# Performance work log

Hardware: AMD Instinct MI355X
Metric: run time of the kernel (lower is better)

## Reference

```python
import jax, jax.numpy as jnp
import numpy as np

N = 50000      # nodes
E = 800000     # edges (before self-loops)
D = 128        # input_dim
H = 128        # hidden_dim
G = 256        # graphs in batch


def setup_inputs() -> dict:
    key = jax.random.key(0)
    ks = jax.random.split(key, 6)
    x = jax.random.normal(ks[0], (N, D), dtype=jnp.float32)
    edge_index = jax.random.randint(ks[1], (2, E), 0, N, dtype=jnp.int32)
    batch = jnp.sort(jax.random.randint(ks[2], (N,), 0, G, dtype=jnp.int32))
    W1 = jax.random.normal(ks[3], (D, H), dtype=jnp.float32) / np.sqrt(D).astype(np.float32)
    b1 = jnp.zeros((H,), jnp.float32)
    W2 = jax.random.normal(ks[4], (H, H), dtype=jnp.float32) / np.sqrt(H).astype(np.float32)
    b2 = jnp.zeros((H,), jnp.float32)
    alpha = jnp.full((H,), 0.25, jnp.float32)  # PReLU(hidden_dim) init
    return dict(x=x, edge_index=edge_index, batch=batch,
                W1=W1, b1=b1, W2=W2, b2=b2, alpha=alpha)


def _gcn_layer(z, W, b, src, dst, norm):
    # GCNConv: z' = D^{-1/2}(A+I)D^{-1/2} (z W) + b
    zw = z @ W                                            # [N,H] dense GEMM
    agg = jnp.zeros_like(zw).at[dst].add(norm[:, None] * zw[src])  # scatter-add over edges
    return agg + b


def reference(x, edge_index, batch, W1, b1, W2, b2, alpha):
    loop = jnp.arange(N, dtype=edge_index.dtype)
    src = jnp.concatenate([edge_index[0], loop])          # add self-loops
    dst = jnp.concatenate([edge_index[1], loop])
    deg = jnp.zeros((N,), x.dtype).at[dst].add(jnp.float32(1.0))
    dinv = jnp.where(deg > 0, jax.lax.rsqrt(deg), 0.0)
    norm = dinv[src] * dinv[dst]                          # [E+N] edge weights

    zs = []
    z = x
    for (W, b) in ((W1, b1), (W2, b2)):
        z = _gcn_layer(z, W, b, src, dst, norm)
        z = jnp.where(z > 0, z, alpha * z)                # channel-wise PReLU (shared)
        zs.append(z)

    gs = [jax.ops.segment_sum(zi, batch, num_segments=G) for zi in zs]  # global_add_pool
    g = jnp.concatenate(gs, axis=1)                       # [G, num_layers*H]
    return z, g
```

## Files before the change

### kernel.cpp

```cpp
#include <hip/hip_runtime.h>
#include <stdint.h>


#define CAP 96

typedef __attribute__((ext_vector_type(8))) short short8;
typedef __attribute__((ext_vector_type(4))) float f32x4;

__device__ __forceinline__ uint16_t bf16rne(float f) {
    uint32_t u = __float_as_uint(f);
    uint32_t r = (u + 0x7fffu + ((u >> 16) & 1u)) >> 16;
    return (uint16_t)r;
}
__device__ __forceinline__ float bf_lo(uint32_t v) { return __uint_as_float(v << 16); }
__device__ __forceinline__ float bf_hi(uint32_t v) { return __uint_as_float(v & 0xffff0000u); }

__global__ __launch_bounds__(512) void k0(int* __restrict__ cursor, int nbC, int N,
                                          const float* __restrict__ W1,
                                          const float* __restrict__ W2,
                                          uint16_t* __restrict__ Wf1,
                                          uint16_t* __restrict__ Wf2,
                                          float* __restrict__ g_out, int nbZ,
                                          uint32_t* __restrict__ zw) {
    int bid = blockIdx.x, t = threadIdx.x;
    if (bid < nbC) {
        int i = bid * 512 + t;
        if (i <= N) cursor[i] = 0;
        if (bid == 0 && t < 64) zw[(size_t)N * 64 + t] = 0u;
    } else if (bid < nbC + 8) {
        int tid = (bid - nbC) * 512 + t;
        const float* W = (tid & 2048) ? W2 : W1;
        uint16_t* O = (tid & 2048) ? Wf2 : Wf1;
        int q16 = tid & 2047;
        int lane = q16 & 63, n0ks = q16 >> 6;
        int n0 = n0ks >> 2, ks = n0ks & 3;
        int m = lane & 15, quad = lane >> 4;
        int nn = n0 * 16 + m;
        int kkb = ks * 32 + quad * 8;
        uint16_t v[8];
#pragma unroll
        for (int j = 0; j < 8; ++j) v[j] = bf16rne(W[(kkb + j) * 128 + nn]);
        *(short8*)&O[q16 * 8] = *(short8*)v;
    } else {
        int idx = (bid - nbC - 8) * 512 + t;
        ((float4*)g_out)[idx] = make_float4(0.f, 0.f, 0.f, 0.f);
    }
}

__device__ __forceinline__ void gemm_body(const float* Xf, const uint16_t* Xb,
                                          const uint16_t* __restrict__ Wf,
                                          uint16_t* __restrict__ Y, int nrows,
                                          const int* __restrict__ cnt,
                                          uint16_t* Wl, int bid, int t) {
    int lane = t & 63, w = t >> 6;
    int row0 = bid * 128;
    for (int c = t; c < 2048; c += 512)
        *(short8*)&Wl[c * 8] = *(const short8*)&Wf[c * 8];
    int m = lane & 15, quad = lane >> 4;
    int arow = row0 + w * 16 + m;
    bool rowok = arow < nrows;
    short8 a[4];
    short8 zer = {0, 0, 0, 0, 0, 0, 0, 0};
    if (Xb) {
        const uint16_t* aptr = Xb + (size_t)arow * 128 + quad * 8;
#pragma unroll
        for (int ks = 0; ks < 4; ++ks)
            a[ks] = rowok ? *(const short8*)(aptr + ks * 32) : zer;
    } else {
        const float* ap = Xf + (size_t)arow * 128 + quad * 8;
#pragma unroll
        for (int ks = 0; ks < 4; ++ks) {
            if (rowok) {
                float4 u0 = *(const float4*)(ap + ks * 32);
                float4 u1 = *(const float4*)(ap + ks * 32 + 4);
                uint32_t q[4];
                q[0] = (uint32_t)bf16rne(u0.x) | ((uint32_t)bf16rne(u0.y) << 16);
                q[1] = (uint32_t)bf16rne(u0.z) | ((uint32_t)bf16rne(u0.w) << 16);
                q[2] = (uint32_t)bf16rne(u1.x) | ((uint32_t)bf16rne(u1.y) << 16);
                q[3] = (uint32_t)bf16rne(u1.z) | ((uint32_t)bf16rne(u1.w) << 16);
                a[ks] = *(short8*)q;
            } else a[ks] = zer;
        }
    }
    __syncthreads();

    f32x4 acc[8];
#pragma unroll
    for (int i = 0; i < 8; ++i) acc[i] = (f32x4){0.f, 0.f, 0.f, 0.f};
#pragma unroll
    for (int ks = 0; ks < 4; ++ks)
#pragma unroll
        for (int n0 = 0; n0 < 8; ++n0) {
            short8 b = *(short8*)&Wl[((n0 * 4 + ks) * 64 + lane) * 8];
            acc[n0] = __builtin_amdgcn_mfma_f32_16x16x32_bf16(a[ks], b, acc[n0], 0, 0, 0);
        }
    __syncthreads();

    float dsc[4] = {1.f, 1.f, 1.f, 1.f};
    if (cnt) {
#pragma unroll
        for (int r = 0; r < 4; ++r) {
            int gr = row0 + w * 16 + quad * 4 + r;
            int d = (gr < nrows) ? cnt[gr] : 0;
            dsc[r] = rsqrtf((float)(d + 1));
        }
    }

    uint16_t* Ep = Wl;
#pragma unroll
    for (int n0 = 0; n0 < 8; ++n0)
#pragma unroll
        for (int r = 0; r < 4; ++r)
            Ep[(w * 16 + quad * 4 + r) * 136 + n0 * 16 + m] = bf16rne(acc[n0][r] * dsc[r]);
    for (int r16 = 0; r16 < 16; ++r16) {
        int row = row0 + w * 16 + r16;
        if (row < nrows) {
            uint32_t v = *(uint32_t*)&Ep[(w * 16 + r16) * 136 + lane * 2];
            ((uint32_t*)Y)[(size_t)row * 64 + lane] = v;
        }
    }
}

__device__ __forceinline__ void fill_body(const int* __restrict__ src, const int* __restrict__ dst,
                                          int* __restrict__ cursor, uint16_t* __restrict__ col,
                                          int E, int fb, int t) {
    int base = fb * 2048 + t;
    int d[4], s[4], p[4];
#pragma unroll
    for (int k = 0; k < 4; ++k) {
        int e = base + k * 512;
        d[k] = (e < E) ? dst[e] : -1;
        s[k] = (e < E) ? src[e] : 0;
    }
#pragma unroll
    for (int k = 0; k < 4; ++k) if (d[k] >= 0) p[k] = atomicAdd(&cursor[d[k]], 1);
#pragma unroll
    for (int k = 0; k < 4; ++k)
        if (d[k] >= 0 && p[k] < CAP) col[(size_t)d[k] * CAP + p[k]] = (uint16_t)s[k];
}

__global__ __launch_bounds__(512, 8) void k5(const float* __restrict__ X,
                                             const uint16_t* __restrict__ Wf,
                                             uint16_t* __restrict__ Y, int nrows, int gemmGrid,
                                             const int* __restrict__ src, const int* __restrict__ dst,
                                             int* __restrict__ cursor, uint16_t* __restrict__ col,
                                             int E, int fillGrid) {
    __shared__ uint16_t Wl[17408];
    int bid = blockIdx.x, t = threadIdx.x;
    int mn = min(gemmGrid, fillGrid), mn2 = 2 * mn;
    int role, idx;
    if (bid < mn2) { role = bid & 1; idx = bid >> 1; }
    else { role = (gemmGrid > fillGrid) ? 0 : 1; idx = bid - mn2 + mn; }
    if (role == 0) gemm_body(X, nullptr, Wf, Y, nrows, nullptr, Wl, idx, t);
    else fill_body(src, dst, cursor, col, E, idx, t);
}

__global__ __launch_bounds__(512, 8) void gemm2k(const uint16_t* __restrict__ Xb,
                                                 const uint16_t* __restrict__ Wf,
                                                 uint16_t* __restrict__ Y, int nrows,
                                                 const int* __restrict__ cnt) {
    __shared__ uint16_t Wl[17408];
    gemm_body(nullptr, Xb, Wf, Y, nrows, cnt, Wl, blockIdx.x, threadIdx.x);
}

template <bool PS>
__global__ __launch_bounds__(256) void aggp(const uint32_t* __restrict__ zw,
                                            const int* __restrict__ cnt,
                                            const uint16_t* __restrict__ col,
                                            const float* __restrict__ bias,
                                            const float* __restrict__ alpha,
                                            const int* __restrict__ batch,
                                            float* __restrict__ gout, int col_off,
                                            uint32_t* __restrict__ z1b,
                                            float* __restrict__ zoutf,
                                            int mode, int n) {
    __shared__ int gsh[4];
    __shared__ float red[4][128];
    int wv = threadIdx.x >> 6;
    int lane = threadIdx.x & 63;
    int node = blockIdx.x * 4 + wv;
    bool valid = node < n;
    int nc = __builtin_amdgcn_readfirstlane(valid ? node : (n - 1));
    int c = lane * 2;
    int deg = cnt[nc];
    float di = rsqrtf((float)(deg + 1));
    uint32_t sv = zw[(size_t)nc * 64 + lane];
    float sw = PS ? 1.f : di;
    float ax = sw * bf_lo(sv), ay = sw * bf_hi(sv);
    float bx = 0.f, by = 0.f;
    int len = min(deg, CAP);
    int len8 = (len + 7) & ~7;
    const uint32_t* cbu = (const uint32_t*)(col + (size_t)nc * CAP);
    uint32_t cc = cbu[lane < 48 ? lane : 0];
    for (int e = 0; e < len8; e += 8) {
        int h = e >> 1;
        uint32_t q0 = (uint32_t)__builtin_amdgcn_readlane((int)cc, h);
        uint32_t q1 = (uint32_t)__builtin_amdgcn_readlane((int)cc, h + 1);
        uint32_t q2 = (uint32_t)__builtin_amdgcn_readlane((int)cc, h + 2);
        uint32_t q3 = (uint32_t)__builtin_amdgcn_readlane((int)cc, h + 3);
        int s0 = (e + 0 < len) ? (int)(q0 & 0xffffu) : n;
        int s1 = (e + 1 < len) ? (int)(q0 >> 16)     : n;
        int s2 = (e + 2 < len) ? (int)(q1 & 0xffffu) : n;
        int s3 = (e + 3 < len) ? (int)(q1 >> 16)     : n;
        int s4 = (e + 4 < len) ? (int)(q2 & 0xffffu) : n;
        int s5 = (e + 5 < len) ? (int)(q2 >> 16)     : n;
        int s6 = (e + 6 < len) ? (int)(q3 & 0xffffu) : n;
        int s7 = (e + 7 < len) ? (int)(q3 >> 16)     : n;
        uint32_t v0 = zw[(size_t)s0 * 64 + lane];
        uint32_t v1 = zw[(size_t)s1 * 64 + lane];
        uint32_t v2 = zw[(size_t)s2 * 64 + lane];
        uint32_t v3 = zw[(size_t)s3 * 64 + lane];
        uint32_t v4 = zw[(size_t)s4 * 64 + lane];
        uint32_t v5 = zw[(size_t)s5 * 64 + lane];
        uint32_t v6 = zw[(size_t)s6 * 64 + lane];
        uint32_t v7 = zw[(size_t)s7 * 64 + lane];
        float w0 = PS ? 1.f : rsqrtf((float)(cnt[s0] + 1));
        float w1 = PS ? 1.f : rsqrtf((float)(cnt[s1] + 1));
        float w2 = PS ? 1.f : rsqrtf((float)(cnt[s2] + 1));
        float w3 = PS ? 1.f : rsqrtf((float)(cnt[s3] + 1));
        float w4 = PS ? 1.f : rsqrtf((float)(cnt[s4] + 1));
        float w5 = PS ? 1.f : rsqrtf((float)(cnt[s5] + 1));
        float w6 = PS ? 1.f : rsqrtf((float)(cnt[s6] + 1));
        float w7 = PS ? 1.f : rsqrtf((float)(cnt[s7] + 1));
        ax += w0 * bf_lo(v0); ay += w0 * bf_hi(v0);
        bx += w1 * bf_lo(v1); by += w1 * bf_hi(v1);
        ax += w2 * bf_lo(v2); ay += w2 * bf_hi(v2);
        bx += w3 * bf_lo(v3); by += w3 * bf_hi(v3);
        ax += w4 * bf_lo(v4); ay += w4 * bf_hi(v4);
        bx += w5 * bf_lo(v5); by += w5 * bf_hi(v5);
        ax += w6 * bf_lo(v6); ay += w6 * bf_hi(v6);
        bx += w7 * bf_lo(v7); by += w7 * bf_hi(v7);
    }
    ax += bx; ay += by;
    float zx = di * ax + bias[c];
    float zy = di * ay + bias[c + 1];
    float px = alpha[c], py = alpha[c + 1];
    zx = zx > 0.f ? zx : px * zx;
    zy = zy > 0.f ? zy : py * zy;

    if (valid) {
        if (mode == 0) {
            uint32_t pk = (uint32_t)bf16rne(zx) | ((uint32_t)bf16rne(zy) << 16);
            z1b[(size_t)nc * 64 + lane] = pk;
        } else {
            ((float2*)zoutf)[(size_t)nc * 64 + lane] = make_float2(zx, zy);
        }
    }

    int g = batch[nc];
    float cx = valid ? zx : 0.f, cy = valid ? zy : 0.f;
    if (lane == 0) gsh[wv] = valid ? g : -1 - wv;
    __syncthreads();
    bool uni = (gsh[0] == gsh[1]) && (gsh[1] == gsh[2]) && (gsh[2] == gsh[3]);
    if (uni) {
        red[wv][c] = cx; red[wv][c + 1] = cy;
        __syncthreads();
        if (wv == 0) {
            float sx = red[0][c] + red[1][c] + red[2][c] + red[3][c];
            float sy = red[0][c + 1] + red[1][c + 1] + red[2][c + 1] + red[3][c + 1];
            float* base = &gout[(size_t)g * 256 + col_off];
            atomicAdd(&base[c], sx);
            atomicAdd(&base[c + 1], sy);
        }
    } else {
        __syncthreads();
        if (valid) {
            float* base = &gout[(size_t)g * 256 + col_off];
            atomicAdd(&base[c], cx);
            atomicAdd(&base[c + 1], cy);
        }
    }
}

extern "C" void kernel_launch(void* const* d_in, const int* in_sizes, int n_in,
                              void* d_out, int out_size, void* d_ws, size_t ws_size,
                              hipStream_t stream) {
    const float* x     = (const float*)d_in[0];
    const int*   eidx  = (const int*)d_in[1];
    const int*   batch = (const int*)d_in[2];
    const float* W1    = (const float*)d_in[3];
    const float* b1    = (const float*)d_in[4];
    const float* W2    = (const float*)d_in[5];
    const float* b2    = (const float*)d_in[6];
    const float* alpha = (const float*)d_in[7];

    const int N = in_sizes[2];
    const int E = in_sizes[1] / 2;
    const int G = (out_size - N * 128) / 256;

    const int* src = eidx;
    const int* dst = eidx + E;

    char* ws = (char*)d_ws;
    size_t off = 0;
    auto alloc = [&](size_t bytes) { void* q = ws + off; off = (off + bytes + 255) & ~(size_t)255; return q; };
    int*      cursor = (int*)alloc((size_t)(N + 1) * 4);
    uint16_t* col    = (uint16_t*)alloc((size_t)N * CAP * 2);
    uint32_t* zw     = (uint32_t*)alloc((size_t)(N + 1) * 128 * 2);
    uint32_t* z1b    = (uint32_t*)alloc((size_t)N * 128 * 2);
    uint16_t* Wf1    = (uint16_t*)alloc(128 * 128 * 2);
    uint16_t* Wf2    = (uint16_t*)alloc(128 * 128 * 2);

    float* z_out = (float*)d_out;
    float* g_out = (float*)d_out + (size_t)N * 128;

    int nbC      = (N + 512) / 512;
    int nbZ      = (G * 256 / 4 + 511) / 512;
    int fillGrid = (E + 2047) / 2048;
    int gemmGrid = (N + 127) / 128;
    int aggGrid  = (N + 3) / 4;

    k0<<<nbC + 8 + nbZ, 512, 0, stream>>>(cursor, nbC, N, W1, W2, Wf1, Wf2, g_out, nbZ, zw);
    k5<<<gemmGrid + fillGrid, 512, 0, stream>>>(x, Wf1, (uint16_t*)zw, N, gemmGrid,
                                                src, dst, cursor, col, E, fillGrid);
    aggp<false><<<aggGrid, 256, 0, stream>>>(zw, cursor, col, b1, alpha, batch,
                                             g_out, 0, z1b, nullptr, 0, N);
    gemm2k<<<gemmGrid, 512, 0, stream>>>((const uint16_t*)z1b, Wf2, (uint16_t*)zw, N, cursor);
    aggp<true><<<aggGrid, 256, 0, stream>>>(zw, cursor, col, b2, alpha, batch,
                                            g_out, 128, nullptr, z_out, 1, N);
}
```

Before: 229.1 us.

## Slice zw feature matrix into four channel planes for cache-local gathers

The GEMM output zw is stored as four column slices of 32 channels, each a contiguous plane, and the aggregation kernel is reorganised so each wave handles 4 nodes with 16 lanes per node over one slice. Block index mapping interleaves slices so each slice's working set (about 3.2 MB) is meant to stay resident in cache during the random neighbour gathers. Column indices are now broadcast via ds_bpermute per 16-lane group instead of readlane. This adds more blocks, divergent loop lengths within a wave (bounded by the max degree of its 4 nodes), and more index and degree loads per channel slice.

```diff
diff --git a/kernel.cpp b/kernel.cpp
--- a/kernel.cpp
+++ b/kernel.cpp
@@ -21,12 +21,13 @@
                                           uint16_t* __restrict__ Wf1,
                                           uint16_t* __restrict__ Wf2,
                                           float* __restrict__ g_out, int nbZ,
-                                          uint32_t* __restrict__ zw) {
+                                          uint32_t* __restrict__ zw, int SL) {
     int bid = blockIdx.x, t = threadIdx.x;
     if (bid < nbC) {
         int i = bid * 512 + t;
         if (i <= N) cursor[i] = 0;
-        if (bid == 0 && t < 64) zw[(size_t)N * 64 + t] = 0u;
+        if (bid == 0 && t < 64)
+            zw[(size_t)(t >> 4) * SL + (size_t)N * 16 + (t & 15)] = 0u;
     } else if (bid < nbC + 8) {
         int tid = (bid - nbC) * 512 + t;
         const float* W = (tid & 2048) ? W2 : W1;
@@ -51,7 +52,7 @@
                                           const uint16_t* __restrict__ Wf,
                                           uint16_t* __restrict__ Y, int nrows,
                                           const int* __restrict__ cnt,
-                                          uint16_t* Wl, int bid, int t) {
+                                          uint16_t* Wl, int bid, int t, int ySL) {
     int lane = t & 63, w = t >> 6;
     int row0 = bid * 128;
     for (int c = t; c < 2048; c += 512)
@@ -116,7 +117,10 @@
         int row = row0 + w * 16 + r16;
         if (row < nrows) {
             uint32_t v = *(uint32_t*)&Ep[(w * 16 + r16) * 136 + lane * 2];
-            ((uint32_t*)Y)[(size_t)row * 64 + lane] = v;
+            if (ySL)
+                ((uint32_t*)Y)[(size_t)(lane >> 4) * ySL + (size_t)row * 16 + (lane & 15)] = v;
+            else
+                ((uint32_t*)Y)[(size_t)row * 64 + lane] = v;
         }
     }
 }
@@ -144,23 +148,23 @@
                                              uint16_t* __restrict__ Y, int nrows, int gemmGrid,
                                              const int* __restrict__ src, const int* __restrict__ dst,
                                              int* __restrict__ cursor, uint16_t* __restrict__ col,
-                                             int E, int fillGrid) {
+                                             int E, int fillGrid, int SL) {
     __shared__ uint16_t Wl[17408];
     int bid = blockIdx.x, t = threadIdx.x;
     int mn = min(gemmGrid, fillGrid), mn2 = 2 * mn;
     int role, idx;
     if (bid < mn2) { role = bid & 1; idx = bid >> 1; }
     else { role = (gemmGrid > fillGrid) ? 0 : 1; idx = bid - mn2 + mn; }
-    if (role == 0) gemm_body(X, nullptr, Wf, Y, nrows, nullptr, Wl, idx, t);
+    if (role == 0) gemm_body(X, nullptr, Wf, Y, nrows, nullptr, Wl, idx, t, SL);
     else fill_body(src, dst, cursor, col, E, idx, t);
 }
 
 __global__ __launch_bounds__(512, 8) void gemm2k(const uint16_t* __restrict__ Xb,
                                                  const uint16_t* __restrict__ Wf,
                                                  uint16_t* __restrict__ Y, int nrows,
-                                                 const int* __restrict__ cnt) {
+                                                 const int* __restrict__ cnt, int SL) {
     __shared__ uint16_t Wl[17408];
-    gemm_body(nullptr, Xb, Wf, Y, nrows, cnt, Wl, blockIdx.x, threadIdx.x);
+    gemm_body(nullptr, Xb, Wf, Y, nrows, cnt, Wl, blockIdx.x, threadIdx.x, SL);
 }
 
 template <bool PS>
@@ -173,101 +177,119 @@
                                             float* __restrict__ gout, int col_off,
                                             uint32_t* __restrict__ z1b,
                                             float* __restrict__ zoutf,
-                                            int mode, int n) {
-    __shared__ int gsh[4];
-    __shared__ float red[4][128];
-    int wv = threadIdx.x >> 6;
-    int lane = threadIdx.x & 63;
-    int node = blockIdx.x * 4 + wv;
+                                            int mode, int n, int SL, int NB) {
+    __shared__ int gsh[16];
+    __shared__ float red[4][32];
+    int bid = blockIdx.x;
+    int s = (bid & 7) >> 1;
+    int j = ((bid >> 3) << 1) | (bid & 1);
+    if (j >= NB) return;
+    int t = threadIdx.x;
+    int wv = t >> 6, lane = t & 63;
+    int g = lane >> 4, i = lane & 15;
+    int node = j * 16 + wv * 4 + g;
     bool valid = node < n;
-    int nc = __builtin_amdgcn_readfirstlane(valid ? node : (n - 1));
-    int c = lane * 2;
-    int deg = cnt[nc];
+    int nd = valid ? node : n;
+    int ncl = valid ? node : (n - 1);
+    const uint32_t* zs = zw + (size_t)s * SL;
+    int deg = cnt[nd];
     float di = rsqrtf((float)(deg + 1));
-    uint32_t sv = zw[(size_t)nc * 64 + lane];
+    uint32_t sv = zs[(uint32_t)nd * 16 + i];
     float sw = PS ? 1.f : di;
     float ax = sw * bf_lo(sv), ay = sw * bf_hi(sv);
     float bx = 0.f, by = 0.f;
     int len = min(deg, CAP);
     int len8 = (len + 7) & ~7;
-    const uint32_t* cbu = (const uint32_t*)(col + (size_t)nc * CAP);
-    uint32_t cc = cbu[lane < 48 ? lane : 0];
-    for (int e = 0; e < len8; e += 8) {
-        int h = e >> 1;
-        uint32_t q0 = (uint32_t)__builtin_amdgcn_readlane((int)cc, h);
-        uint32_t q1 = (uint32_t)__builtin_amdgcn_readlane((int)cc, h + 1);
-        uint32_t q2 = (uint32_t)__builtin_amdgcn_readlane((int)cc, h + 2);
-        uint32_t q3 = (uint32_t)__builtin_amdgcn_readlane((int)cc, h + 3);
-        int s0 = (e + 0 < len) ? (int)(q0 & 0xffffu) : n;
-        int s1 = (e + 1 < len) ? (int)(q0 >> 16)     : n;
-        int s2 = (e + 2 < len) ? (int)(q1 & 0xffffu) : n;
-        int s3 = (e + 3 < len) ? (int)(q1 >> 16)     : n;
-        int s4 = (e + 4 < len) ? (int)(q2 & 0xffffu) : n;
-        int s5 = (e + 5 < len) ? (int)(q2 >> 16)     : n;
-        int s6 = (e + 6 < len) ? (int)(q3 & 0xffffu) : n;
-        int s7 = (e + 7 < len) ? (int)(q3 >> 16)     : n;
-        uint32_t v0 = zw[(size_t)s0 * 64 + lane];
-        uint32_t v1 = zw[(size_t)s1 * 64 + lane];
-        uint32_t v2 = zw[(size_t)s2 * 64 + lane];
-        uint32_t v3 = zw[(size_t)s3 * 64 + lane];
-        uint32_t v4 = zw[(size_t)s4 * 64 + lane];
-        uint32_t v5 = zw[(size_t)s5 * 64 + lane];
-        uint32_t v6 = zw[(size_t)s6 * 64 + lane];
-        uint32_t v7 = zw[(size_t)s7 * 64 + lane];
-        float w0 = PS ? 1.f : rsqrtf((float)(cnt[s0] + 1));
-        float w1 = PS ? 1.f : rsqrtf((float)(cnt[s1] + 1));
-        float w2 = PS ? 1.f : rsqrtf((float)(cnt[s2] + 1));
-        float w3 = PS ? 1.f : rsqrtf((float)(cnt[s3] + 1));
-        float w4 = PS ? 1.f : rsqrtf((float)(cnt[s4] + 1));
-        float w5 = PS ? 1.f : rsqrtf((float)(cnt[s5] + 1));
-        float w6 = PS ? 1.f : rsqrtf((float)(cnt[s6] + 1));
-        float w7 = PS ? 1.f : rsqrtf((float)(cnt[s7] + 1));
-        ax += w0 * bf_lo(v0); ay += w0 * bf_hi(v0);
-        bx += w1 * bf_lo(v1); by += w1 * bf_hi(v1);
-        ax += w2 * bf_lo(v2); ay += w2 * bf_hi(v2);
-        bx += w3 * bf_lo(v3); by += w3 * bf_hi(v3);
-        ax += w4 * bf_lo(v4); ay += w4 * bf_hi(v4);
-        bx += w5 * bf_lo(v5); by += w5 * bf_hi(v5);
-        ax += w6 * bf_lo(v6); ay += w6 * bf_hi(v6);
-        bx += w7 * bf_lo(v7); by += w7 * bf_hi(v7);
+    int m1 = max(len8, __shfl_xor(len8, 16));
+    int mx = __builtin_amdgcn_readfirstlane(max(m1, __shfl_xor(m1, 32)));
+    int permbase = (lane & 48) << 2;
+    const uint32_t* cbu = (const uint32_t*)col;
+
+    for (int c0 = 0; c0 < mx; c0 += 32) {
+        uint32_t cc = cbu[(uint32_t)ncl * (CAP / 2) + (c0 >> 1) + i];
+        int top = min(mx - c0, 32);
+        for (int e = 0; e < top; e += 8) {
+            uint32_t q0 = (uint32_t)__builtin_amdgcn_ds_bpermute(permbase + (((e + 0) >> 1) << 2), (int)cc);
+            uint32_t q1 = (uint32_t)__builtin_amdgcn_ds_bpermute(permbase + (((e + 2) >> 1) << 2), (int)cc);
+            uint32_t q2 = (uint32_t)__builtin_amdgcn_ds_bpermute(permbase + (((e + 4) >> 1) << 2), (int)cc);
+            uint32_t q3 = (uint32_t)__builtin_amdgcn_ds_bpermute(permbase + (((e + 6) >> 1) << 2), (int)cc);
+            int jj = c0 + e;
+            int s0 = (jj + 0 < len) ? (int)(q0 & 0xffffu) : n;
+            int s1 = (jj + 1 < len) ? (int)(q0 >> 16)     : n;
+            int s2 = (jj + 2 < len) ? (int)(q1 & 0xffffu) : n;
+            int s3 = (jj + 3 < len) ? (int)(q1 >> 16)     : n;
+            int s4 = (jj + 4 < len) ? (int)(q2 & 0xffffu) : n;
+            int s5 = (jj + 5 < len) ? (int)(q2 >> 16)     : n;
+            int s6 = (jj + 6 < len) ? (int)(q3 & 0xffffu) : n;
+            int s7 = (jj + 7 < len) ? (int)(q3 >> 16)     : n;
+            uint32_t v0 = zs[(uint32_t)s0 * 16 + i];
+            uint32_t v1 = zs[(uint32_t)s1 * 16 + i];
+            uint32_t v2 = zs[(uint32_t)s2 * 16 + i];
+            uint32_t v3 = zs[(uint32_t)s3 * 16 + i];
+            uint32_t v4 = zs[(uint32_t)s4 * 16 + i];
+            uint32_t v5 = zs[(uint32_t)s5 * 16 + i];
+            uint32_t v6 = zs[(uint32_t)s6 * 16 + i];
+            uint32_t v7 = zs[(uint32_t)s7 * 16 + i];
+            float w0 = PS ? 1.f : rsqrtf((float)(cnt[s0] + 1));
+            float w1 = PS ? 1.f : rsqrtf((float)(cnt[s1] + 1));
+            float w2 = PS ? 1.f : rsqrtf((float)(cnt[s2] + 1));
+            float w3 = PS ? 1.f : rsqrtf((float)(cnt[s3] + 1));
+            float w4 = PS ? 1.f : rsqrtf((float)(cnt[s4] + 1));
+            float w5 = PS ? 1.f : rsqrtf((float)(cnt[s5] + 1));
+            float w6 = PS ? 1.f : rsqrtf((float)(cnt[s6] + 1));
+            float w7 = PS ? 1.f : rsqrtf((float)(cnt[s7] + 1));
+            ax += w0 * bf_lo(v0); ay += w0 * bf_hi(v0);
+            bx += w1 * bf_lo(v1); by += w1 * bf_hi(v1);
+            ax += w2 * bf_lo(v2); ay += w2 * bf_hi(v2);
+            bx += w3 * bf_lo(v3); by += w3 * bf_hi(v3);
+            ax += w4 * bf_lo(v4); ay += w4 * bf_hi(v4);
+            bx += w5 * bf_lo(v5); by += w5 * bf_hi(v5);
+            ax += w6 * bf_lo(v6); ay += w6 * bf_hi(v6);
+            bx += w7 * bf_lo(v7); by += w7 * bf_hi(v7);
+        }
     }
     ax += bx; ay += by;
-    float zx = di * ax + bias[c];
-    float zy = di * ay + bias[c + 1];
-    float px = alpha[c], py = alpha[c + 1];
-    zx = zx > 0.f ? zx : px * zx;
-    zy = zy > 0.f ? zy : py * zy;
+    float2 bb = ((const float2*)bias)[s * 16 + i];
+    float2 aa = ((const float2*)alpha)[s * 16 + i];
+    float zx = di * ax + bb.x;
+    float zy = di * ay + bb.y;
+    zx = zx > 0.f ? zx : aa.x * zx;
+    zy = zy > 0.f ? zy : aa.y * zy;
 
     if (valid) {
         if (mode == 0) {
             uint32_t pk = (uint32_t)bf16rne(zx) | ((uint32_t)bf16rne(zy) << 16);
-            z1b[(size_t)nc * 64 + lane] = pk;
+            z1b[(size_t)node * 64 + s * 16 + i] = pk;
         } else {
-            ((float2*)zoutf)[(size_t)nc * 64 + lane] = make_float2(zx, zy);
-        }
-    }
-
-    int g = batch[nc];
+            ((float2*)zoutf)[(size_t)node * 64 + s * 16 + i] = make_float2(zx, zy);
+        }
+    }
+
+    int gr = valid ? batch[nd] : -1;
+    if (i == 0) gsh[wv * 4 + g] = gr;
+    __syncthreads();
+    int g0 = gsh[0];
+    bool uni = true;
+#pragma unroll
+    for (int q = 1; q < 16; ++q) uni &= (gsh[q] == g0);
     float cx = valid ? zx : 0.f, cy = valid ? zy : 0.f;
-    if (lane == 0) gsh[wv] = valid ? g : -1 - wv;
-    __syncthreads();
-    bool uni = (gsh[0] == gsh[1]) && (gsh[1] == gsh[2]) && (gsh[2] == gsh[3]);
     if (uni) {
-        red[wv][c] = cx; red[wv][c + 1] = cy;
+        float r1x = cx + __shfl_xor(cx, 16), r1y = cy + __shfl_xor(cy, 16);
+        float r2x = r1x + __shfl_xor(r1x, 32), r2y = r1y + __shfl_xor(r1y, 32);
+        if (lane < 16) { red[wv][2 * i] = r2x; red[wv][2 * i + 1] = r2y; }
         __syncthreads();
-        if (wv == 0) {
-            float sx = red[0][c] + red[1][c] + red[2][c] + red[3][c];
-            float sy = red[0][c + 1] + red[1][c + 1] + red[2][c + 1] + red[3][c + 1];
-            float* base = &gout[(size_t)g * 256 + col_off];
-            atomicAdd(&base[c], sx);
-            atomicAdd(&base[c + 1], sy);
+        if (wv == 0 && lane < 16) {
+            float sx = red[0][2 * i] + red[1][2 * i] + red[2][2 * i] + red[3][2 * i];
+            float sy = red[0][2 * i + 1] + red[1][2 * i + 1] + red[2][2 * i + 1] + red[3][2 * i + 1];
+            float* base = &gout[(size_t)g0 * 256 + col_off + s * 32 + 2 * i];
+            atomicAdd(&base[0], sx);
+            atomicAdd(&base[1], sy);
         }
     } else {
-        __syncthreads();
         if (valid) {
-            float* base = &gout[(size_t)g * 256 + col_off];
-            atomicAdd(&base[c], cx);
-            atomicAdd(&base[c + 1], cy);
+            float* base = &gout[(size_t)gr * 256 + col_off + s * 32 + 2 * i];
+            atomicAdd(&base[0], cx);
+            atomicAdd(&base[1], cy);
         }
     }
 }
@@ -304,18 +326,21 @@
     float* z_out = (float*)d_out;
     float* g_out = (float*)d_out + (size_t)N * 128;
 
+    const int SL = (N + 1) * 16;
     int nbC      = (N + 512) / 512;
     int nbZ      = (G * 256 / 4 + 511) / 512;
     int fillGrid = (E + 2047) / 2048;
     int gemmGrid = (N + 127) / 128;
-    int aggGrid  = (N + 3) / 4;
-
-    k0<<<nbC + 8 + nbZ, 512, 0, stream>>>(cursor, nbC, N, W1, W2, Wf1, Wf2, g_out, nbZ, zw);
+    int NB       = (N + 15) / 16;
+    int NBpad    = (NB + 1) & ~1;
+    int aggGrid  = NBpad * 4;
+
+    k0<<<nbC + 8 + nbZ, 512, 0, stream>>>(cursor, nbC, N, W1, W2, Wf1, Wf2, g_out, nbZ, zw, SL);
     k5<<<gemmGrid + fillGrid, 512, 0, stream>>>(x, Wf1, (uint16_t*)zw, N, gemmGrid,
-                                                src, dst, cursor, col, E, fillGrid);
+                                                src, dst, cursor, col, E, fillGrid, SL);
     aggp<false><<<aggGrid, 256, 0, stream>>>(zw, cursor, col, b1, alpha, batch,
-                                             g_out, 0, z1b, nullptr, 0, N);
-    gemm2k<<<gemmGrid, 512, 0, stream>>>((const uint16_t*)z1b, Wf2, (uint16_t*)zw, N, cursor);
+                                             g_out, 0, z1b, nullptr, 0, N, SL, NB);
+    gemm2k<<<gemmGrid, 512, 0, stream>>>((const uint16_t*)z1b, Wf2, (uint16_t*)zw, N, cursor, SL);
     aggp<true><<<aggGrid, 256, 0, stream>>>(zw, cursor, col, b2, alpha, batch,
-                                            g_out, 128, nullptr, z_out, 1, N);
-}
+                                            g_out, 128, nullptr, z_out, 1, N, SL, NB);
+}
```

Measured after the change: 244.9 us. +6.9%, slower.
